# Kernel tuning notes

Measured on AMD Instinct MI355X. Metric: run time of the kernel, lower is better.

Reference implementation:

```python
import jax, jax.numpy as jnp
import numpy as np

V = 1024  # codebook size
D = 256   # embedding dim


def setup_inputs() -> dict:
    key = jax.random.key(0)
    k1, k2, k3 = jax.random.split(key, 3)
    logits = jax.random.normal(k1, (16, 64, 64, V), dtype=jnp.float32)
    target_indices = jax.random.randint(k2, (16, 64, 64), 0, V, dtype=jnp.int64)
    codebook = jax.random.normal(k3, (V, D), dtype=jnp.float32)
    return {"logits": logits, "target_indices": target_indices, "codebook": codebook}


def reference(logits, target_indices, codebook):
    # Handle (B, C, H, W) channel-first layout like the torch module.
    if logits.ndim == 4 and logits.shape[1] == codebook.shape[0]:
        logits = jnp.transpose(logits, (0, 2, 3, 1))
    logits_flat = logits.reshape(-1, logits.shape[-1])        # [N, V]
    targets_flat = target_indices.reshape(-1)                 # [N]
    n_samples = logits_flat.shape[0]

    probs = jax.nn.softmax(logits_flat, axis=-1)              # [N, V]
    pred_vectors = jnp.einsum('nv,vd->nd', probs, codebook)   # [N, D]
    target_vectors = codebook[targets_flat]                   # [N, D] gather
    diff = pred_vectors - target_vectors
    total_loss = jnp.sum(diff * diff)
    return total_loss / (n_samples * codebook.shape[1])
```

## Files before the change

### kernel.cpp

```cpp
#include <hip/hip_runtime.h>

typedef __bf16 bf16_t;
typedef bf16_t v8bf __attribute__((ext_vector_type(8)));
typedef bf16_t v4bf __attribute__((ext_vector_type(4)));
typedef float v16f __attribute__((ext_vector_type(16)));

#define NV 1024
#define ND 256
#define NR 65536
#define BM 32

__global__ void prep_codebook(const float* __restrict__ cb, bf16_t* __restrict__ cws) {
    int g = blockIdx.x * blockDim.x + threadIdx.x;
    int e = g * 4;
#pragma unroll
    for (int ii = 0; ii < 4; ++ii, ++e) {
        int kt = e >> 12;
        int d  = (e >> 4) & 255;
        int ki = e & 15;
        cws[e] = (bf16_t)cb[(kt * 16 + ki) * ND + d];
    }
}

__device__ inline v4bf exp4(float4 x, float& s) {
    v4bf e;
    e[0] = (bf16_t)__expf(x.x);
    e[1] = (bf16_t)__expf(x.y);
    e[2] = (bf16_t)__expf(x.z);
    e[3] = (bf16_t)__expf(x.w);
    s += (float)e[0] + (float)e[1] + (float)e[2] + (float)e[3];
    return e;
}

__global__ __launch_bounds__(256, 2)
void scl_main(const float* __restrict__ logits,
              const int* __restrict__ targets,
              const float* __restrict__ cbf,
              const bf16_t* __restrict__ cws,
              float* __restrict__ out) {
    __shared__ char sE[BM * 2048];
    __shared__ float sSum[BM];

    const int tid  = (int)threadIdx.x;
    const int w    = tid >> 6;
    const int l    = tid & 63;
    const int brow = (int)blockIdx.x * BM;

#pragma unroll 2
    for (int rr = 0; rr < 8; ++rr) {
        const int r = w * 8 + rr;
        const float4* rowp = (const float4*)(logits + (size_t)(brow + r) * NV);
        float4 x0 = rowp[l];
        float4 x1 = rowp[l + 64];
        float4 x2 = rowp[l + 128];
        float4 x3 = rowp[l + 192];
        float s = 0.f;
        v4bf e0 = exp4(x0, s);
        v4bf e1 = exp4(x1, s);
        v4bf e2 = exp4(x2, s);
        v4bf e3 = exp4(x3, s);
        char* rbase = sE + r * 2048;
        const int sw = (r & 7) << 4;
        *(v4bf*)(rbase + ((8 * l +    0) ^ sw)) = e0;
        *(v4bf*)(rbase + ((8 * l +  512) ^ sw)) = e1;
        *(v4bf*)(rbase + ((8 * l + 1024) ^ sw)) = e2;
        *(v4bf*)(rbase + ((8 * l + 1536) ^ sw)) = e3;
#pragma unroll
        for (int off = 32; off > 0; off >>= 1)
            s += __shfl_xor(s, off, 64);
        if (l == 0) sSum[r] = s;
    }
    __syncthreads();

    const int rA  = l & 31;
    const int g8  = l >> 5;
    const int swA = (rA & 7) << 4;
    const char* aBase = sE + rA * 2048;
    const int cb0 = w << 6;
    const bf16_t* bBase = cws + (size_t)(cb0 + (l & 31)) * 16 + g8 * 8;

    v16f acc0 = {0,0,0,0,0,0,0,0,0,0,0,0,0,0,0,0};
    v16f acc1 = {0,0,0,0,0,0,0,0,0,0,0,0,0,0,0,0};

#pragma unroll 4
    for (int kt = 0; kt < 64; ++kt) {
        const int koff = ((kt << 5) | (g8 << 4)) ^ swA;
        v8bf a  = *(const v8bf*)(aBase + koff);
        v8bf b0 = *(const v8bf*)(bBase + kt * 4096);
        v8bf b1 = *(const v8bf*)(bBase + kt * 4096 + 512);
        acc0 = __builtin_amdgcn_mfma_f32_32x32x16_bf16(a, b0, acc0, 0, 0, 0);
        acc1 = __builtin_amdgcn_mfma_f32_32x32x16_bf16(a, b1, acc1, 0, 0, 0);
    }

    float local = 0.f;
    const int c0 = cb0 + (l & 31);
    const int rb4 = (l >> 5) << 2;
#pragma unroll
    for (int q = 0; q < 16; ++q) {
        const int rloc = (q & 3) + ((q >> 2) << 3) + rb4;
        const int grow = brow + rloc;
        const float rs = __builtin_amdgcn_rcpf(sSum[rloc]);
        const int tgt  = targets[grow];
        const float* cr = cbf + (size_t)tgt * ND;
        float d0 = acc0[q] * rs - cr[c0];
        float d1 = acc1[q] * rs - cr[c0 + 32];
        local = fmaf(d0, d0, fmaf(d1, d1, local));
    }
#pragma unroll
    for (int off = 32; off > 0; off >>= 1)
        local += __shfl_xor(local, off, 64);
    if (l == 0)
        atomicAdd(out, local * (1.0f / (65536.0f * 256.0f)));
}

extern "C" void kernel_launch(void* const* d_in, const int* in_sizes, int n_in,
                              void* d_out, int out_size, void* d_ws, size_t ws_size,
                              hipStream_t stream) {
    const float* logits  = (const float*)d_in[0];
    const int*   targets = (const int*)d_in[1];
    const float* cbf     = (const float*)d_in[2];

    bf16_t* cws = (bf16_t*)d_ws;
    float*  out = (float*)d_out;

    hipMemsetAsync(d_out, 0, sizeof(float), stream);
    prep_codebook<<<256, 256, 0, stream>>>(cbf, cws);
    scl_main<<<2048, 256, 0, stream>>>(logits, targets, cbf, cws, out);
}
```

Baseline: 442.1 us.

## Stream logits in double-buffered K chunks overlapping loads with MFMA

```diff
diff --git a/kernel.cpp b/kernel.cpp
--- a/kernel.cpp
+++ b/kernel.cpp
@@ -9,17 +9,20 @@
 #define ND 256
 #define NR 65536
 #define BM 32
+#define KC 256
+#define CT 16
+#define NCH 4
 
 __global__ void prep_codebook(const float* __restrict__ cb, bf16_t* __restrict__ cws) {
-    int g = blockIdx.x * blockDim.x + threadIdx.x;
-    int e = g * 4;
-#pragma unroll
-    for (int ii = 0; ii < 4; ++ii, ++e) {
-        int kt = e >> 12;
-        int d  = (e >> 4) & 255;
-        int ki = e & 15;
-        cws[e] = (bf16_t)cb[(kt * 16 + ki) * ND + d];
-    }
+    int g  = blockIdx.x * blockDim.x + threadIdx.x;
+    int v  = g >> 6;
+    int d0 = (g & 63) * 4;
+    const float4 x = *(const float4*)(cb + v * ND + d0);
+    bf16_t* base = cws + (v >> 4) * 4096 + (v & 15);
+    base[(d0 + 0) * 16] = (bf16_t)x.x;
+    base[(d0 + 1) * 16] = (bf16_t)x.y;
+    base[(d0 + 2) * 16] = (bf16_t)x.z;
+    base[(d0 + 3) * 16] = (bf16_t)x.w;
 }
 
 __device__ inline v4bf exp4(float4 x, float& s) {
@@ -32,13 +35,13 @@
     return e;
 }
 
-__global__ __launch_bounds__(256, 2)
+__global__ __launch_bounds__(256, 4)
 void scl_main(const float* __restrict__ logits,
               const int* __restrict__ targets,
               const float* __restrict__ cbf,
               const bf16_t* __restrict__ cws,
               float* __restrict__ out) {
-    __shared__ char sE[BM * 2048];
+    __shared__ char  sE[2][BM * 512];
     __shared__ float sSum[BM];
 
     const int tid  = (int)threadIdx.x;
@@ -46,54 +49,62 @@
     const int l    = tid & 63;
     const int brow = (int)blockIdx.x * BM;
 
-#pragma unroll 2
-    for (int rr = 0; rr < 8; ++rr) {
-        const int r = w * 8 + rr;
-        const float4* rowp = (const float4*)(logits + (size_t)(brow + r) * NV);
-        float4 x0 = rowp[l];
-        float4 x1 = rowp[l + 64];
-        float4 x2 = rowp[l + 128];
-        float4 x3 = rowp[l + 192];
-        float s = 0.f;
-        v4bf e0 = exp4(x0, s);
-        v4bf e1 = exp4(x1, s);
-        v4bf e2 = exp4(x2, s);
-        v4bf e3 = exp4(x3, s);
-        char* rbase = sE + r * 2048;
-        const int sw = (r & 7) << 4;
-        *(v4bf*)(rbase + ((8 * l +    0) ^ sw)) = e0;
-        *(v4bf*)(rbase + ((8 * l +  512) ^ sw)) = e1;
-        *(v4bf*)(rbase + ((8 * l + 1024) ^ sw)) = e2;
-        *(v4bf*)(rbase + ((8 * l + 1536) ^ sw)) = e3;
-#pragma unroll
-        for (int off = 32; off > 0; off >>= 1)
-            s += __shfl_xor(s, off, 64);
-        if (l == 0) sSum[r] = s;
-    }
-    __syncthreads();
+    float4 st[8];
+    float  srow[8] = {0, 0, 0, 0, 0, 0, 0, 0};
 
     const int rA  = l & 31;
     const int g8  = l >> 5;
     const int swA = (rA & 7) << 4;
-    const char* aBase = sE + rA * 2048;
     const int cb0 = w << 6;
     const bf16_t* bBase = cws + (size_t)(cb0 + (l & 31)) * 16 + g8 * 8;
 
     v16f acc0 = {0,0,0,0,0,0,0,0,0,0,0,0,0,0,0,0};
     v16f acc1 = {0,0,0,0,0,0,0,0,0,0,0,0,0,0,0,0};
 
+#pragma unroll
+    for (int rr = 0; rr < 8; ++rr)
+        st[rr] = ((const float4*)(logits + (size_t)(brow + w * 8 + rr) * NV))[l];
+
+    for (int c = 0; c < NCH; ++c) {
+        char* buf = sE[c & 1];
+#pragma unroll
+        for (int rr = 0; rr < 8; ++rr) {
+            const int r = w * 8 + rr;
+            v4bf e = exp4(st[rr], srow[rr]);
+            *(v4bf*)(buf + r * 512 + ((l * 8) ^ ((r & 7) << 4))) = e;
+        }
+        if (c < NCH - 1) {
+#pragma unroll
+            for (int rr = 0; rr < 8; ++rr)
+                st[rr] = ((const float4*)(logits +
+                          (size_t)(brow + w * 8 + rr) * NV + (c + 1) * KC))[l];
+        }
+        __syncthreads();
+        const char* aBase = buf + rA * 512;
 #pragma unroll 4
-    for (int kt = 0; kt < 64; ++kt) {
-        const int koff = ((kt << 5) | (g8 << 4)) ^ swA;
-        v8bf a  = *(const v8bf*)(aBase + koff);
-        v8bf b0 = *(const v8bf*)(bBase + kt * 4096);
-        v8bf b1 = *(const v8bf*)(bBase + kt * 4096 + 512);
-        acc0 = __builtin_amdgcn_mfma_f32_32x32x16_bf16(a, b0, acc0, 0, 0, 0);
-        acc1 = __builtin_amdgcn_mfma_f32_32x32x16_bf16(a, b1, acc1, 0, 0, 0);
+        for (int ktl = 0; ktl < CT; ++ktl) {
+            const int kt   = c * CT + ktl;
+            const int koff = ((ktl << 5) | (g8 << 4)) ^ swA;
+            v8bf a  = *(const v8bf*)(aBase + koff);
+            v8bf b0 = *(const v8bf*)(bBase + (size_t)kt * 4096);
+            v8bf b1 = *(const v8bf*)(bBase + (size_t)kt * 4096 + 512);
+            acc0 = __builtin_amdgcn_mfma_f32_32x32x16_bf16(a, b0, acc0, 0, 0, 0);
+            acc1 = __builtin_amdgcn_mfma_f32_32x32x16_bf16(a, b1, acc1, 0, 0, 0);
+        }
     }
 
+#pragma unroll
+    for (int rr = 0; rr < 8; ++rr) {
+        float s = srow[rr];
+#pragma unroll
+        for (int off = 32; off > 0; off >>= 1)
+            s += __shfl_xor(s, off, 64);
+        if (l == 0) sSum[w * 8 + rr] = s;
+    }
+    __syncthreads();
+
     float local = 0.f;
-    const int c0 = cb0 + (l & 31);
+    const int c0  = cb0 + (l & 31);
     const int rb4 = (l >> 5) << 2;
 #pragma unroll
     for (int q = 0; q < 16; ++q) {
```

Result: slower. 484.3 us (+9.5%).
